# Kernel tuning notes

Measured on AMD Instinct MI355X. Metric: run time of the kernel, lower is better.

Reference implementation:

```python
import jax, jax.numpy as jnp
import numpy as np

B, S, D = 16, 2048, 128

def setup_inputs() -> dict:
    key = jax.random.key(0)
    kq, kk, kv, km = jax.random.split(key, 4)
    Q = jax.random.normal(kq, (B, S, D), dtype=jnp.float32)
    K = jax.random.normal(kk, (B, S, D), dtype=jnp.float32)
    V = jax.random.normal(kv, (B, S, D), dtype=jnp.float32)
    # mask: True entries are masked out (filled with -inf), same as torch.masked_fill_
    mask = jax.random.randint(km, (B, S, S), 0, 2).astype(bool)
    return {"Q": Q, "K": K, "V": V, "mask": mask, "dk": 128}

def reference(Q, K, V, mask, dk):
    # scores: [B, S_q, S_k]
    w = jnp.einsum('bqd,bkd->bqk', Q, K)
    w = jnp.where(mask, -jnp.inf, w)
    # scale applied to masked scores (as in original: mask first, then divide);
    # -inf / scale stays -inf, so math matches exactly.
    scale = jnp.asarray(dk, w.dtype) ** 0.5
    p = jax.nn.softmax(w / scale, axis=-1)
    # context: [B, S_q, D]
    return jnp.einsum('bqk,bkd->bqd', p, V)
```

## Files before the change

### kernel.cpp

```cpp
#include <hip/hip_runtime.h>
#include <hip/hip_bf16.h>
#include <stdint.h>

typedef __attribute__((ext_vector_type(8)))  short short8;
typedef __attribute__((ext_vector_type(4)))  float floatx4;
typedef __attribute__((ext_vector_type(16))) float floatx16;

#define S_LEN 2048
#define DH    128
#define BQ    64
#define BKV   64
#define NSTEP (S_LEN / BKV)
#define SCALE 0.08838834764831845f
#define SCALE2 0.12753785429791905f
#define DTHR 11.541560327111708f

__device__ __forceinline__ float ex2(float x) { return __builtin_amdgcn_exp2f(x); }

__device__ __forceinline__ unsigned short f2b(float f) {
    union { float f; unsigned u; } v; v.f = f;
    unsigned r = v.u + 0x7fffu + ((v.u >> 16) & 1u);
    return (unsigned short)(r >> 16);
}

__device__ __forceinline__ unsigned cvt_pk(float lo, float hi) {
    unsigned r;
    asm("v_cvt_pk_bf16_f32 %0, %1, %2" : "=v"(r) : "v"(lo), "v"(hi));
    return r;
}

__device__ __forceinline__ void gll16(const void* g, void* l) {
    __builtin_amdgcn_global_load_lds(
        (__attribute__((address_space(1))) void*)(g),
        (__attribute__((address_space(3))) void*)(l), 16, 0, 0);
}


__global__ __launch_bounds__(256) void conv_k(const float* __restrict__ K,
                                              unsigned short* __restrict__ Kbf)
{
    int i = blockIdx.x * 256 + threadIdx.x;
    float4 v = ((const float4*)K)[i];
    ushort4 o;
    o.x = f2b(v.x); o.y = f2b(v.y); o.z = f2b(v.z); o.w = f2b(v.w);
    ((ushort4*)Kbf)[i] = o;
}

__global__ __launch_bounds__(256) void transp_v(const float* __restrict__ V,
                                                unsigned short* __restrict__ Vt)
{
    __shared__ float t[32][33];
    const int k0 = blockIdx.x * 32, d0 = blockIdx.y * 32, b = blockIdx.z;
    const int tx = threadIdx.x & 31, ty = threadIdx.x >> 5;
    const float* Vb = V + ((size_t)b * S_LEN + k0) * DH + d0;
    #pragma unroll
    for (int i = 0; i < 4; ++i)
        t[ty + 8 * i][tx] = Vb[(size_t)(ty + 8 * i) * DH + tx];
    __syncthreads();
    unsigned short* Vtb = Vt + ((size_t)b * DH + d0) * S_LEN + k0;
    #pragma unroll
    for (int i = 0; i < 4; ++i)
        Vtb[(size_t)(ty + 8 * i) * S_LEN + tx] = f2b(t[tx][ty + 8 * i]);
}

__global__ __launch_bounds__(256) void pack_mask(const int* __restrict__ M,
                                                 unsigned long long* __restrict__ P)
{
    const int lane = threadIdx.x & 63;
    const int wv   = threadIdx.x >> 6;
    const int row  = blockIdx.x * 4 + wv;
    const int* Mr  = M + (size_t)row * S_LEN;
    unsigned long long* Pr = P + (size_t)row * 32;
    #pragma unroll
    for (int it = 0; it < 8; ++it) {
        int4 v = *(const int4*)(Mr + it * 256 + lane * 4);
        unsigned long long b0 = __ballot(v.x != 0);
        unsigned long long b1 = __ballot(v.y != 0);
        unsigned long long b2 = __ballot(v.z != 0);
        unsigned long long b3 = __ballot(v.w != 0);
        if (lane == 0) {
            Pr[it * 4 + 0] = b0;
            Pr[it * 4 + 1] = b1;
            Pr[it * 4 + 2] = b2;
            Pr[it * 4 + 3] = b3;
        }
    }
}

#define LDS_BYTES 69632

__global__ __launch_bounds__(256, 2)
void attn_fwd(const float* __restrict__ Q, const unsigned short* __restrict__ Kbf,
              const unsigned short* __restrict__ Vt,
              const unsigned long long* __restrict__ Pm,
              float* __restrict__ O)
{
    __shared__ __align__(128) char lds[LDS_BYTES];

    const int tid  = threadIdx.x;
    const int lane = tid & 63;
    const int w    = tid >> 6;
    const int wq   = w & 1;
    const int wk   = w >> 1;
    const int lq   = lane & 31;
    const int hi   = lane >> 5;
    const int qt   = blockIdx.x;
    const int b    = blockIdx.y;
    const int q0   = qt * BQ;

    const int vd = tid & 127;
    const int vh = tid >> 7;
    const int krow_l = lane >> 4;
    const int kcol_l = (lane & 15) * 16;

    short8 qf[8];
    {
        const float* qrow = Q + ((size_t)(b * S_LEN + q0 + wq * 32 + lq)) * DH;
        #pragma unroll
        for (int dsub = 0; dsub < 8; ++dsub) {
            const float* p = qrow + dsub * 16 + hi * 8;
            float4 a  = *(const float4*)(p);
            float4 bb = *(const float4*)(p + 4);
            short8 f;
            f[0] = f2b(a.x * SCALE2);  f[1] = f2b(a.y * SCALE2);
            f[2] = f2b(a.z * SCALE2);  f[3] = f2b(a.w * SCALE2);
            f[4] = f2b(bb.x * SCALE2); f[5] = f2b(bb.y * SCALE2);
            f[6] = f2b(bb.z * SCALE2); f[7] = f2b(bb.w * SCALE2);
            qf[dsub] = f;
        }
    }

    float m_run = -1e30f;
    float l_run = 0.f;
    floatx16 accO[4];
    #pragma unroll
    for (int i = 0; i < 4; ++i) accO[i] = (floatx16)(0.f);

    const char*           Kb8 = (const char*)(Kbf + (size_t)b * S_LEN * DH);
    const unsigned short* Vtb = Vt + (size_t)b * DH * S_LEN;
    const unsigned long long* Pk = Pm
        + ((size_t)(b * S_LEN + q0 + wq * 32 + lq) << 5);

    short8 vreg[4];
    unsigned long long mgc[4], mgn[4];

#define LOAD_MG(DST, G) {                                                     \
    ulonglong2 a_ = *(const ulonglong2*)(Pk + (G) * 4);                       \
    ulonglong2 b_ = *(const ulonglong2*)(Pk + (G) * 4 + 2);                   \
    DST[0] = a_.x; DST[1] = a_.y; DST[2] = b_.x; DST[3] = b_.y; }

    #pragma unroll
    for (int i = 0; i < 4; ++i) {
        int j = (w << 2) | i;
        int r = 4 * j + krow_l;
        unsigned cb = (unsigned)kcol_l ^ (unsigned)((r & 15) << 4);
        gll16(Kb8 + (size_t)r * 256 + cb, lds + j * 1024);
    }
    #pragma unroll
    for (int j = 0; j < 4; ++j)
        vreg[j] = *(const short8*)(Vtb + (size_t)vd * S_LEN + vh * 32 + j * 8);
    #pragma unroll
    for (int j = 0; j < 4; ++j)
        *(short8*)(lds + 32768 + vd * 144 + vh * 64 + j * 16) = vreg[j];
    #pragma unroll
    for (int j = 0; j < 4; ++j)
        vreg[j] = *(const short8*)(Vtb + (size_t)vd * S_LEN + BKV + vh * 32 + j * 8);
    LOAD_MG(mgc, 0);
    LOAD_MG(mgn, 1);
    __syncthreads();

#define STEP_BODY(T, TT) {                                                    \
    const int pb  = (T) & 1;                                                  \
    const int kv0 = (T) * BKV;                                                \
                                                  \
    if ((T) + 1 < NSTEP) {                                                    \
        const char* Ksrc = Kb8 + (size_t)(kv0 + BKV) * 256;                   \
        char* KHn = lds + ((pb ^ 1) * 16384);                                 \
        _Pragma("unroll")                                                     \
        for (int i = 0; i < 4; ++i) {                                         \
            int j = (w << 2) | i;                                             \
            int r = 4 * j + krow_l;                                           \
            unsigned cb = (unsigned)kcol_l ^ (unsigned)((r & 15) << 4);       \
            gll16(Ksrc + (size_t)r * 256 + cb, KHn + j * 1024);               \
        }                                                                     \
    }                                                                         \
                            \
    if ((T) + 1 < NSTEP) {                                                    \
        _Pragma("unroll")                                                     \
        for (int j = 0; j < 4; ++j)                                           \
            *(short8*)(lds + 32768 + (pb ^ 1) * 18432 + vd * 144 + vh * 64    \
                       + j * 16) = vreg[j];                                   \
    }                                                                         \
    if ((T) + 2 < NSTEP) {                                                    \
        const unsigned short* vs_ = Vtb + (size_t)vd * S_LEN                  \
                                   + (kv0 + 2 * BKV) + vh * 32;               \
        _Pragma("unroll")                                                     \
        for (int j = 0; j < 4; ++j)                                           \
            vreg[j] = *(const short8*)(vs_ + j * 8);                          \
    }                                                                         \
            \
    floatx16 accS = (floatx16)(0.f);                                          \
    {                                                                         \
        const char* KHp = lds + pb * 16384;                                   \
        const int krow = wk * 32 + lq;                                        \
        const char* kbase = KHp + krow * 256;                                 \
        const unsigned ksw = (unsigned)((krow & 15) << 4);                    \
        __builtin_amdgcn_s_setprio(1);                                        \
        _Pragma("unroll")                                                     \
        for (int dsub = 0; dsub < 8; ++dsub) {                                \
            short8 kf = *(const short8*)(kbase +                              \
                ((unsigned)(dsub * 32 + hi * 16) ^ ksw));                     \
            accS = __builtin_amdgcn_mfma_f32_32x32x16_bf16(                   \
                       kf, qf[dsub], accS, 0, 0, 0);                          \
        }                                                                     \
        __builtin_amdgcn_s_setprio(0);                                        \
    }                                                                         \
                               \
    const int base_ = (TT) * 16 + wk * 8 + hi;                                \
    unsigned mb0 = (unsigned)(mgc[0] >> base_);                               \
    unsigned mb1 = (unsigned)(mgc[1] >> base_);                               \
    unsigned mb2 = (unsigned)(mgc[2] >> base_);                               \
    unsigned mb3 = (unsigned)(mgc[3] >> base_);                               \
    float p_[16];                                                             \
    _Pragma("unroll")                                                         \
    for (int j = 0; j < 4; ++j) {                                             \
        p_[4*j+0] = ((mb0 >> (2*j)) & 1u) ? -1e30f : accS[4*j+0];             \
        p_[4*j+1] = ((mb1 >> (2*j)) & 1u) ? -1e30f : accS[4*j+1];             \
        p_[4*j+2] = ((mb2 >> (2*j)) & 1u) ? -1e30f : accS[4*j+2];             \
        p_[4*j+3] = ((mb3 >> (2*j)) & 1u) ? -1e30f : accS[4*j+3];             \
    }                                                                         \
    float mx = p_[0];                                                         \
    _Pragma("unroll")                                                         \
    for (int r = 1; r < 16; ++r) mx = fmaxf(mx, p_[r]);                       \
    mx = fmaxf(mx, __shfl_xor(mx, 32));                                       \
    int need = __any(mx - m_run > DTHR);                                      \
    float corr = 1.0f;                                                        \
    if (need) {                                                               \
        float mn = fmaxf(m_run, mx);                                          \
        corr = ex2(m_run - mn);                                               \
        m_run = mn;                                                           \
    }                                                                         \
    float ts = 0.f;                                                           \
    _Pragma("unroll")                                                         \
    for (int r = 0; r < 16; ++r) { p_[r] = ex2(p_[r] - m_run); ts += p_[r]; } \
    ts += __shfl_xor(ts, 32);                                                 \
    if (need) {                                                               \
        l_run = l_run * corr + ts;                                            \
        _Pragma("unroll")                                                     \
        for (int ds = 0; ds < 4; ++ds) {                                      \
            floatx16 o = accO[ds];                                            \
            _Pragma("unroll")                                                 \
            for (int r = 0; r < 16; ++r) o[r] *= corr;                        \
            accO[ds] = o;                                                     \
        }                                                                     \
    } else {                                                                  \
        l_run += ts;                                                          \
    }                                                                         \
              \
    short8 pf[2];                                                             \
    _Pragma("unroll")                                                         \
    for (int ks = 0; ks < 2; ++ks) {                                          \
        unsigned a01 = cvt_pk(p_[8*ks+0], p_[8*ks+1]);                        \
        unsigned a23 = cvt_pk(p_[8*ks+2], p_[8*ks+3]);                        \
        unsigned b01 = cvt_pk(p_[8*ks+4], p_[8*ks+5]);                        \
        unsigned b23 = cvt_pk(p_[8*ks+6], p_[8*ks+7]);                        \
        unsigned ta01 = (unsigned)__shfl_xor((int)a01, 32);                   \
        unsigned ta23 = (unsigned)__shfl_xor((int)a23, 32);                   \
        unsigned tb01 = (unsigned)__shfl_xor((int)b01, 32);                   \
        unsigned tb23 = (unsigned)__shfl_xor((int)b23, 32);                   \
        union { unsigned u[4]; short8 v; } pu;                                \
        pu.u[0] = hi ? tb01 : a01;                                            \
        pu.u[1] = hi ? tb23 : a23;                                            \
        pu.u[2] = hi ? b01 : ta01;                                            \
        pu.u[3] = hi ? b23 : ta23;                                            \
        pf[ks] = pu.v;                                                        \
    }                                                                         \
           \
    {                                                                         \
        const char* VTp = lds + 32768 + pb * 18432;                           \
        __builtin_amdgcn_s_setprio(1);                                        \
        _Pragma("unroll")                                                     \
        for (int ds = 0; ds < 4; ++ds) {                                      \
            const char* vbase = VTp + (ds * 32 + lq) * 144 + wk * 64 + hi*16; \
            _Pragma("unroll")                                                 \
            for (int ks = 0; ks < 2; ++ks) {                                  \
                short8 vf = *(const short8*)(vbase + ks * 32);                \
                accO[ds] = __builtin_amdgcn_mfma_f32_32x32x16_bf16(           \
                               vf, pf[ks], accO[ds], 0, 0, 0);                \
            }                                                                 \
        }                                                                     \
        __builtin_amdgcn_s_setprio(0);                                        \
    }                                                                         \
    __syncthreads(); }

    for (int g = 0; g < 8; ++g) {
        STEP_BODY(4 * g + 0, 0)
        STEP_BODY(4 * g + 1, 1)
        STEP_BODY(4 * g + 2, 2)
        STEP_BODY(4 * g + 3, 3)
        mgc[0] = mgn[0]; mgc[1] = mgn[1]; mgc[2] = mgn[2]; mgc[3] = mgn[3];
        if (g + 2 < 8) LOAD_MG(mgn, g + 2);
    }
#undef STEP_BODY
#undef LOAD_MG

    {
        float* mg = (float*)lds;
        const int slot = (wq * 64 + lane) * 68;
        if (wk == 1) {
            #pragma unroll
            for (int ds = 0; ds < 4; ++ds)
                #pragma unroll
                for (int rr = 0; rr < 4; ++rr) {
                    float4 v;
                    v.x = accO[ds][4*rr+0]; v.y = accO[ds][4*rr+1];
                    v.z = accO[ds][4*rr+2]; v.w = accO[ds][4*rr+3];
                    *(float4*)(mg + slot + ds * 16 + rr * 4) = v;
                }
            mg[slot + 64] = m_run;
            mg[slot + 65] = l_run;
        }
        __syncthreads();
        if (wk == 0) {
            float m1 = mg[slot + 64], l1 = mg[slot + 65];
            float m  = fmaxf(m_run, m1);
            float f0 = ex2(m_run - m), f1 = ex2(m1 - m);
            float l  = l_run * f0 + l1 * f1;
            float inv = (l > 0.f) ? 1.f / l : 0.f;
            float* Ob = O + ((size_t)(b * S_LEN + q0 + wq * 32 + lq)) * DH;
            #pragma unroll
            for (int ds = 0; ds < 4; ++ds)
                #pragma unroll
                for (int rr = 0; rr < 4; ++rr) {
                    float4 part = *(const float4*)(mg + slot + ds * 16 + rr * 4);
                    float4 ov;
                    ov.x = (accO[ds][4*rr+0] * f0 + part.x * f1) * inv;
                    ov.y = (accO[ds][4*rr+1] * f0 + part.y * f1) * inv;
                    ov.z = (accO[ds][4*rr+2] * f0 + part.z * f1) * inv;
                    ov.w = (accO[ds][4*rr+3] * f0 + part.w * f1) * inv;
                    *(float4*)(Ob + ds * 32 + 8 * rr + 4 * hi) = ov;
                }
        }
    }
}

#define FB_LDS_BYTES 77824

__global__ __launch_bounds__(256, 2)
void attn_fwd_fb(const float* __restrict__ Q, const float* __restrict__ K,
                 const float* __restrict__ V, const int* __restrict__ M,
                 float* __restrict__ O)
{
    __shared__ __align__(128) char lds[FB_LDS_BYTES];

    const int tid  = threadIdx.x;
    const int lane = tid & 63;
    const int w    = tid >> 6;
    const int c    = lane & 15;
    const int g    = lane >> 4;
    const int qt   = blockIdx.x;
    const int b    = blockIdx.y;
    const int q0   = qt * 64;

    const int rbase = tid >> 5;
    const int c4    = tid & 31;
    const unsigned swk = (unsigned)(c4 * 8) ^ (unsigned)(rbase << 4);
    const int vd    = tid & 127;
    const int vk0   = (tid >> 7) * 32;

    short8 qf[4];
    {
        const float* qrow = Q + ((size_t)(b * S_LEN + q0 + w * 16 + c)) * DH;
        #pragma unroll
        for (int dk = 0; dk < 4; ++dk) {
            const float* p = qrow + dk * 32 + g * 8;
            float4 a  = *(const float4*)(p);
            float4 bb = *(const float4*)(p + 4);
            short8 f;
            f[0] = f2b(a.x * SCALE);  f[1] = f2b(a.y * SCALE);
            f[2] = f2b(a.z * SCALE);  f[3] = f2b(a.w * SCALE);
            f[4] = f2b(bb.x * SCALE); f[5] = f2b(bb.y * SCALE);
            f[6] = f2b(bb.z * SCALE); f[7] = f2b(bb.w * SCALE);
            qf[dk] = f;
        }
    }

    float m_run[4] = {-1e30f, -1e30f, -1e30f, -1e30f};
    float l_run[4] = {0.f, 0.f, 0.f, 0.f};
    floatx4 accO[8];
    #pragma unroll
    for (int i = 0; i < 8; ++i) accO[i] = (floatx4)(0.f);

    const float* Kb = K + (size_t)b * S_LEN * DH;
    const float* Vb = V + (size_t)b * S_LEN * DH;
    const int*   Mb = M + (size_t)b * S_LEN * S_LEN + (size_t)q0 * S_LEN;

    size_t moff[4];
    #pragma unroll
    for (int r = 0; r < 4; ++r)
        moff[r] = (size_t)(w * 16 + 4 * g + r) * S_LEN;

    float4 kreg[8];
    float  vreg[32];
    int    mreg[16];

    #pragma unroll
    for (int i = 0; i < 8; ++i)
        kreg[i] = *(const float4*)(Kb + (size_t)(i * 8 + rbase) * DH + c4 * 4);
    #pragma unroll
    for (int j = 0; j < 32; ++j)
        vreg[j] = Vb[(size_t)(vk0 + j) * DH + vd];
    #pragma unroll
    for (int r = 0; r < 4; ++r)
        #pragma unroll
        for (int n = 0; n < 4; ++n)
            mreg[r * 4 + n] = Mb[moff[r] + n * 16 + c];

    #pragma unroll
    for (int i = 0; i < 8; ++i) {
        float4 kv = kreg[i];
        unsigned long long kp =
              (unsigned long long)f2b(kv.x)
            | ((unsigned long long)f2b(kv.y) << 16)
            | ((unsigned long long)f2b(kv.z) << 32)
            | ((unsigned long long)f2b(kv.w) << 48);
        *(unsigned long long*)(lds + (i * 8 + rbase) * 256 + swk) = kp;
    }
    {
        char* vbase = lds + 32768 + vd * 144 + vk0 * 2;
        #pragma unroll
        for (int i = 0; i < 4; ++i) {
            short8 pk;
            #pragma unroll
            for (int e = 0; e < 8; ++e) pk[e] = f2b(vreg[i * 8 + e]);
            *(short8*)(vbase + i * 16) = pk;
        }
    }
    #pragma unroll
    for (int i = 0; i < 8; ++i)
        kreg[i] = *(const float4*)(Kb + (size_t)(BKV + i * 8 + rbase) * DH + c4 * 4);
    #pragma unroll
    for (int j = 0; j < 32; ++j)
        vreg[j] = Vb[(size_t)(BKV + vk0 + j) * DH + vd];

    __syncthreads();

    char* psw = lds + 69632 + w * 2048;

    for (int step = 0; step < NSTEP; ++step) {
        const int p = step & 1;
        const int kv0 = step * BKV;
        char* KHp = lds + p * 16384;
        char* VTp = lds + 32768 + p * 18432;

        floatx4 accS[4];
        #pragma unroll
        for (int n = 0; n < 4; ++n) accS[n] = (floatx4)(0.f);
        #pragma unroll
        for (int n = 0; n < 4; ++n) {
            const char* krow = KHp + (n * 16 + c) * 256;
            #pragma unroll
            for (int dk = 0; dk < 4; ++dk) {
                unsigned colb = (unsigned)(dk * 64 + g * 16) ^ (unsigned)((c & 7) << 4);
                short8 kf = *(const short8*)(krow + colb);
                accS[n] = __builtin_amdgcn_mfma_f32_16x16x32_bf16(qf[dk], kf, accS[n], 0, 0, 0);
            }
        }

        float pv[4][4];
        float corr[4];
        #pragma unroll
        for (int r = 0; r < 4; ++r) {
            float sv[4];
            #pragma unroll
            for (int n = 0; n < 4; ++n) {
                float s = accS[n][r];
                if (mreg[r * 4 + n]) s = -1e30f;
                sv[n] = s;
            }
            float tm = fmaxf(fmaxf(sv[0], sv[1]), fmaxf(sv[2], sv[3]));
            #pragma unroll
            for (int off = 1; off < 16; off <<= 1)
                tm = fmaxf(tm, __shfl_xor(tm, off, 64));
            float mn = fmaxf(m_run[r], tm);
            corr[r]  = __expf(m_run[r] - mn);
            m_run[r] = mn;
            float ts = 0.f;
            #pragma unroll
            for (int n = 0; n < 4; ++n) { pv[n][r] = __expf(sv[n] - mn); ts += pv[n][r]; }
            #pragma unroll
            for (int off = 1; off < 16; off <<= 1)
                ts += __shfl_xor(ts, off, 64);
            l_run[r] = l_run[r] * corr[r] + ts;
        }
        if (step + 1 < NSTEP) {
            const int kvn = kv0 + BKV;
            #pragma unroll
            for (int r = 0; r < 4; ++r)
                #pragma unroll
                for (int n = 0; n < 4; ++n)
                    mreg[r * 4 + n] = Mb[moff[r] + kvn + n * 16 + c];
        }

        #pragma unroll
        for (int s8 = 0; s8 < 8; ++s8) {
            floatx4 o = accO[s8];
            o[0] *= corr[0]; o[1] *= corr[1]; o[2] *= corr[2]; o[3] *= corr[3];
            accO[s8] = o;
        }

        #pragma unroll
        for (int r = 0; r < 4; ++r) {
            int rl = 4 * g + r;
            #pragma unroll
            for (int n = 0; n < 4; ++n) {
                unsigned colb = (unsigned)((n * 16 + c) * 2) ^ (unsigned)((rl & 7) << 4);
                *(unsigned short*)(psw + rl * 128 + colb) = f2b(pv[n][r]);
            }
        }

        #pragma unroll
        for (int sub = 0; sub < 2; ++sub) {
            unsigned colb = (unsigned)(sub * 64 + g * 16) ^ (unsigned)((c & 7) << 4);
            short8 pf = *(const short8*)(psw + c * 128 + colb);
            #pragma unroll
            for (int s8 = 0; s8 < 8; ++s8) {
                short8 vf = *(const short8*)(VTp + (s8 * 16 + c) * 144 + sub * 64 + g * 16);
                accO[s8] = __builtin_amdgcn_mfma_f32_16x16x32_bf16(pf, vf, accO[s8], 0, 0, 0);
            }
        }

        if (step + 1 < NSTEP) {
            char* KHn = lds + (p ^ 1) * 16384;
            char* VTn = lds + 32768 + (p ^ 1) * 18432;
            #pragma unroll
            for (int i = 0; i < 8; ++i) {
                float4 kv = kreg[i];
                unsigned long long kp =
                      (unsigned long long)f2b(kv.x)
                    | ((unsigned long long)f2b(kv.y) << 16)
                    | ((unsigned long long)f2b(kv.z) << 32)
                    | ((unsigned long long)f2b(kv.w) << 48);
                *(unsigned long long*)(KHn + (i * 8 + rbase) * 256 + swk) = kp;
            }
            char* vbase = VTn + vd * 144 + vk0 * 2;
            #pragma unroll
            for (int i = 0; i < 4; ++i) {
                short8 pk;
                #pragma unroll
                for (int e = 0; e < 8; ++e) pk[e] = f2b(vreg[i * 8 + e]);
                *(short8*)(vbase + i * 16) = pk;
            }
            if (step + 2 < NSTEP) {
                const int kvn2 = kv0 + 2 * BKV;
                #pragma unroll
                for (int i = 0; i < 8; ++i)
                    kreg[i] = *(const float4*)(Kb + (size_t)(kvn2 + i * 8 + rbase) * DH + c4 * 4);
                #pragma unroll
                for (int j = 0; j < 32; ++j)
                    vreg[j] = Vb[(size_t)(kvn2 + vk0 + j) * DH + vd];
            }
        }
        __syncthreads();
    }

    float inv[4];
    #pragma unroll
    for (int r = 0; r < 4; ++r) inv[r] = (l_run[r] > 0.f) ? 1.f / l_run[r] : 0.f;
    float* Ob = O + ((size_t)(b * S_LEN + q0 + w * 16)) * DH;
    #pragma unroll
    for (int s8 = 0; s8 < 8; ++s8) {
        #pragma unroll
        for (int r = 0; r < 4; ++r) {
            Ob[(size_t)(4 * g + r) * DH + s8 * 16 + c] = accO[s8][r] * inv[r];
        }
    }
}

extern "C" void kernel_launch(void* const* d_in, const int* in_sizes, int n_in,
                              void* d_out, int out_size, void* d_ws, size_t ws_size,
                              hipStream_t stream) {
    const float* Q = (const float*)d_in[0];
    const float* K = (const float*)d_in[1];
    const float* V = (const float*)d_in[2];
    const int*   M = (const int*)d_in[3];
    float*       O = (float*)d_out;

    const size_t elems    = (size_t)16 * S_LEN * DH;
    const size_t kv_bytes = elems * sizeof(unsigned short);
    const size_t pm_bytes = (size_t)16 * S_LEN * 32 * 8;
    if (ws_size >= 2 * kv_bytes + pm_bytes) {
        unsigned short*     Kbf = (unsigned short*)d_ws;
        unsigned short*     Vt  = (unsigned short*)d_ws + elems;
        unsigned long long* Pm  = (unsigned long long*)((char*)d_ws + 2 * kv_bytes);
        conv_k<<<dim3((unsigned)(elems / 4 / 256)), dim3(256), 0, stream>>>(K, Kbf);
        transp_v<<<dim3(S_LEN / 32, DH / 32, 16), dim3(256), 0, stream>>>(V, Vt);
        pack_mask<<<dim3(16 * S_LEN / 4), dim3(256), 0, stream>>>(M, Pm);
        attn_fwd<<<dim3(S_LEN / BQ, 16), dim3(256), 0, stream>>>(Q, Kbf, Vt, Pm, O);
    } else {
        attn_fwd_fb<<<dim3(S_LEN / 64, 16), dim3(256), 0, stream>>>(Q, K, V, M, O);
    }
}
```

Measured before the change: 136.6 us.

## Pre-swizzle K and V into MFMA fragment layout and load directly to registers

The preprocessing kernels now write K and V in bf16, already arranged in the per-lane MFMA operand fragment order. The attention kernel loads these fragments straight from global memory into registers, with K double-buffered across steps. This removes the LDS staging buffers and the per-step __syncthreads, and halves the LDS footprint. In exchange, register pressure rises, the global (L2) fragment loads are now exposed inside the step, and each wave re-reads K/V fragments that were previously shared through LDS.

```diff
diff --git a/kernel.cpp b/kernel.cpp
--- a/kernel.cpp
+++ b/kernel.cpp
@@ -29,25 +29,28 @@
     return r;
 }
 
-__device__ __forceinline__ void gll16(const void* g, void* l) {
-    __builtin_amdgcn_global_load_lds(
-        (__attribute__((address_space(1))) void*)(g),
-        (__attribute__((address_space(3))) void*)(l), 16, 0, 0);
-}
-
-
-__global__ __launch_bounds__(256) void conv_k(const float* __restrict__ K,
-                                              unsigned short* __restrict__ Kbf)
+
+__global__ __launch_bounds__(256) void kfrag_make(const float* __restrict__ K,
+                                                  unsigned short* __restrict__ KF)
 {
-    int i = blockIdx.x * 256 + threadIdx.x;
-    float4 v = ((const float4*)K)[i];
-    ushort4 o;
-    o.x = f2b(v.x); o.y = f2b(v.y); o.z = f2b(v.z); o.w = f2b(v.w);
-    ((ushort4*)Kbf)[i] = o;
-}
-
-__global__ __launch_bounds__(256) void transp_v(const float* __restrict__ V,
-                                                unsigned short* __restrict__ Vt)
+    const int T = blockIdx.x, b = blockIdx.y;
+    const float* Kb = K + ((size_t)b * S_LEN + T * 64) * DH;
+    unsigned short* out = KF + ((size_t)(b * 32 + T)) * 1024 * 8;
+    #pragma unroll
+    for (int i = 0; i < 4; ++i) {
+        int F = i * 256 + threadIdx.x;
+        int lq = F & 31, h = (F >> 5) & 1, dsub = (F >> 6) & 7, wk = F >> 9;
+        const float* src = Kb + (size_t)(wk * 32 + lq) * DH + dsub * 16 + h * 8;
+        float4 a = *(const float4*)src, bb = *(const float4*)(src + 4);
+        short8 f;
+        f[0] = f2b(a.x);  f[1] = f2b(a.y);  f[2] = f2b(a.z);  f[3] = f2b(a.w);
+        f[4] = f2b(bb.x); f[5] = f2b(bb.y); f[6] = f2b(bb.z); f[7] = f2b(bb.w);
+        *(short8*)(out + (size_t)F * 8) = f;
+    }
+}
+
+__global__ __launch_bounds__(256) void vfrag_make(const float* __restrict__ V,
+                                                  unsigned short* __restrict__ VF)
 {
     __shared__ float t[32][33];
     const int k0 = blockIdx.x * 32, d0 = blockIdx.y * 32, b = blockIdx.z;
@@ -57,10 +60,19 @@
     for (int i = 0; i < 4; ++i)
         t[ty + 8 * i][tx] = Vb[(size_t)(ty + 8 * i) * DH + tx];
     __syncthreads();
-    unsigned short* Vtb = Vt + ((size_t)b * DH + d0) * S_LEN + k0;
-    #pragma unroll
-    for (int i = 0; i < 4; ++i)
-        Vtb[(size_t)(ty + 8 * i) * S_LEN + tx] = f2b(t[tx][ty + 8 * i]);
+    if (threadIdx.x < 128) {
+        const int lq = threadIdx.x & 31;
+        const int h  = (threadIdx.x >> 5) & 1;
+        const int ks = threadIdx.x >> 6;
+        const int T = k0 >> 6, wk = (k0 >> 5) & 1, ds = d0 >> 5;
+        short8 f;
+        #pragma unroll
+        for (int e = 0; e < 8; ++e)
+            f[e] = f2b(t[ks * 16 + h * 8 + e][lq]);
+        unsigned short* o = VF +
+            ((((((size_t)(b * 32 + T) * 4 + ds) * 2 + wk) * 2 + ks) * 2 + h) * 32 + lq) * 8;
+        *(short8*)o = f;
+    }
 }
 
 __global__ __launch_bounds__(256) void pack_mask(const int* __restrict__ M,
@@ -87,11 +99,11 @@
     }
 }
 
-#define LDS_BYTES 69632
+#define LDS_BYTES 34816
 
 __global__ __launch_bounds__(256, 2)
-void attn_fwd(const float* __restrict__ Q, const unsigned short* __restrict__ Kbf,
-              const unsigned short* __restrict__ Vt,
+void attn_fwd(const float* __restrict__ Q, const unsigned short* __restrict__ KF,
+              const unsigned short* __restrict__ VF,
               const unsigned long long* __restrict__ Pm,
               float* __restrict__ O)
 {
@@ -108,11 +120,6 @@
     const int b    = blockIdx.y;
     const int q0   = qt * BQ;
 
-    const int vd = tid & 127;
-    const int vh = tid >> 7;
-    const int krow_l = lane >> 4;
-    const int kcol_l = (lane & 15) * 16;
-
     short8 qf[8];
     {
         const float* qrow = Q + ((size_t)(b * S_LEN + q0 + wq * 32 + lq)) * DH;
@@ -136,86 +143,54 @@
     #pragma unroll
     for (int i = 0; i < 4; ++i) accO[i] = (floatx16)(0.f);
 
-    const char*           Kb8 = (const char*)(Kbf + (size_t)b * S_LEN * DH);
-    const unsigned short* Vtb = Vt + (size_t)b * DH * S_LEN;
+    const unsigned short* KFl = KF + (((size_t)(b * 32) * 2 + wk) * 512
+                                      + (size_t)hi * 32 + lq) * 8;
+    const unsigned short* VFl = VF + ((((size_t)(b * 32) * 4 * 2 + wk) * 2) * 2 * 32
+                                      + (size_t)hi * 32 + lq) * 8;
+
     const unsigned long long* Pk = Pm
         + ((size_t)(b * S_LEN + q0 + wq * 32 + lq) << 5);
 
-    short8 vreg[4];
     unsigned long long mgc[4], mgn[4];
+    short8 kfA[8], kfB[8], vfc[8];
 
 #define LOAD_MG(DST, G) {                                                     \
     ulonglong2 a_ = *(const ulonglong2*)(Pk + (G) * 4);                       \
     ulonglong2 b_ = *(const ulonglong2*)(Pk + (G) * 4 + 2);                   \
     DST[0] = a_.x; DST[1] = a_.y; DST[2] = b_.x; DST[3] = b_.y; }
 
-    #pragma unroll
-    for (int i = 0; i < 4; ++i) {
-        int j = (w << 2) | i;
-        int r = 4 * j + krow_l;
-        unsigned cb = (unsigned)kcol_l ^ (unsigned)((r & 15) << 4);
-        gll16(Kb8 + (size_t)r * 256 + cb, lds + j * 1024);
-    }
-    #pragma unroll
-    for (int j = 0; j < 4; ++j)
-        vreg[j] = *(const short8*)(Vtb + (size_t)vd * S_LEN + vh * 32 + j * 8);
-    #pragma unroll
-    for (int j = 0; j < 4; ++j)
-        *(short8*)(lds + 32768 + vd * 144 + vh * 64 + j * 16) = vreg[j];
-    #pragma unroll
-    for (int j = 0; j < 4; ++j)
-        vreg[j] = *(const short8*)(Vtb + (size_t)vd * S_LEN + BKV + vh * 32 + j * 8);
+#define LOAD_KF(DST, T) {                                                     \
+    const unsigned short* kp_ = KFl + (size_t)(T) * (2 * 512 * 8);            \
+    _Pragma("unroll")                                                         \
+    for (int dsub = 0; dsub < 8; ++dsub)                                      \
+        DST[dsub] = *(const short8*)(kp_ + dsub * 512);                       \
+}
+
+#define LOAD_VF(T) {                                                          \
+    _Pragma("unroll")                                                         \
+    for (int ds = 0; ds < 4; ++ds)                                            \
+        _Pragma("unroll")                                                     \
+        for (int ks = 0; ks < 2; ++ks)                                        \
+            vfc[ds * 2 + ks] = *(const short8*)(VFl                           \
+                + ((size_t)(T) * 16 + ds * 4 + ks) * (2 * 32 * 8));           \
+}
+
+    LOAD_KF(kfA, 0);
     LOAD_MG(mgc, 0);
     LOAD_MG(mgn, 1);
-    __syncthreads();
-
-#define STEP_BODY(T, TT) {                                                    \
-    const int pb  = (T) & 1;                                                  \
-    const int kv0 = (T) * BKV;                                                \
-                                                  \
-    if ((T) + 1 < NSTEP) {                                                    \
-        const char* Ksrc = Kb8 + (size_t)(kv0 + BKV) * 256;                   \
-        char* KHn = lds + ((pb ^ 1) * 16384);                                 \
-        _Pragma("unroll")                                                     \
-        for (int i = 0; i < 4; ++i) {                                         \
-            int j = (w << 2) | i;                                             \
-            int r = 4 * j + krow_l;                                           \
-            unsigned cb = (unsigned)kcol_l ^ (unsigned)((r & 15) << 4);       \
-            gll16(Ksrc + (size_t)r * 256 + cb, KHn + j * 1024);               \
-        }                                                                     \
-    }                                                                         \
-                            \
-    if ((T) + 1 < NSTEP) {                                                    \
-        _Pragma("unroll")                                                     \
-        for (int j = 0; j < 4; ++j)                                           \
-            *(short8*)(lds + 32768 + (pb ^ 1) * 18432 + vd * 144 + vh * 64    \
-                       + j * 16) = vreg[j];                                   \
-    }                                                                         \
-    if ((T) + 2 < NSTEP) {                                                    \
-        const unsigned short* vs_ = Vtb + (size_t)vd * S_LEN                  \
-                                   + (kv0 + 2 * BKV) + vh * 32;               \
-        _Pragma("unroll")                                                     \
-        for (int j = 0; j < 4; ++j)                                           \
-            vreg[j] = *(const short8*)(vs_ + j * 8);                          \
-    }                                                                         \
-            \
+
+#define STEP_BODY(T, TT, KFC, KFN) {                                          \
+    if ((T) + 1 < NSTEP) LOAD_KF(KFN, (T) + 1);                               \
+    LOAD_VF(T);                                                               \
+                                                                    \
     floatx16 accS = (floatx16)(0.f);                                          \
-    {                                                                         \
-        const char* KHp = lds + pb * 16384;                                   \
-        const int krow = wk * 32 + lq;                                        \
-        const char* kbase = KHp + krow * 256;                                 \
-        const unsigned ksw = (unsigned)((krow & 15) << 4);                    \
-        __builtin_amdgcn_s_setprio(1);                                        \
-        _Pragma("unroll")                                                     \
-        for (int dsub = 0; dsub < 8; ++dsub) {                                \
-            short8 kf = *(const short8*)(kbase +                              \
-                ((unsigned)(dsub * 32 + hi * 16) ^ ksw));                     \
-            accS = __builtin_amdgcn_mfma_f32_32x32x16_bf16(                   \
-                       kf, qf[dsub], accS, 0, 0, 0);                          \
-        }                                                                     \
-        __builtin_amdgcn_s_setprio(0);                                        \
-    }                                                                         \
-                               \
+    __builtin_amdgcn_s_setprio(1);                                            \
+    _Pragma("unroll")                                                         \
+    for (int dsub = 0; dsub < 8; ++dsub)                                      \
+        accS = __builtin_amdgcn_mfma_f32_32x32x16_bf16(                       \
+                   KFC[dsub], qf[dsub], accS, 0, 0, 0);                       \
+    __builtin_amdgcn_s_setprio(0);                                            \
+                                           \
     const int base_ = (TT) * 16 + wk * 8 + hi;                                \
     unsigned mb0 = (unsigned)(mgc[0] >> base_);                               \
     unsigned mb1 = (unsigned)(mgc[1] >> base_);                               \
@@ -256,7 +231,7 @@
     } else {                                                                  \
         l_run += ts;                                                          \
     }                                                                         \
-              \
+                                 \
     short8 pf[2];                                                             \
     _Pragma("unroll")                                                         \
     for (int ks = 0; ks < 2; ++ks) {                                          \
@@ -275,33 +250,28 @@
         pu.u[3] = hi ? b23 : ta23;                                            \
         pf[ks] = pu.v;                                                        \
     }                                                                         \
-           \
-    {                                                                         \
-        const char* VTp = lds + 32768 + pb * 18432;                           \
-        __builtin_amdgcn_s_setprio(1);                                        \
+                                                                      \
+    __builtin_amdgcn_s_setprio(1);                                            \
+    _Pragma("unroll")                                                         \
+    for (int ds = 0; ds < 4; ++ds)                                            \
         _Pragma("unroll")                                                     \
-        for (int ds = 0; ds < 4; ++ds) {                                      \
-            const char* vbase = VTp + (ds * 32 + lq) * 144 + wk * 64 + hi*16; \
-            _Pragma("unroll")                                                 \
-            for (int ks = 0; ks < 2; ++ks) {                                  \
-                short8 vf = *(const short8*)(vbase + ks * 32);                \
-                accO[ds] = __builtin_amdgcn_mfma_f32_32x32x16_bf16(           \
-                               vf, pf[ks], accO[ds], 0, 0, 0);                \
-            }                                                                 \
-        }                                                                     \
-        __builtin_amdgcn_s_setprio(0);                                        \
-    }                                                                         \
-    __syncthreads(); }
+        for (int ks = 0; ks < 2; ++ks)                                        \
+            accO[ds] = __builtin_amdgcn_mfma_f32_32x32x16_bf16(               \
+                           vfc[ds * 2 + ks], pf[ks], accO[ds], 0, 0, 0);      \
+    __builtin_amdgcn_s_setprio(0);                                            \
+}
 
     for (int g = 0; g < 8; ++g) {
-        STEP_BODY(4 * g + 0, 0)
-        STEP_BODY(4 * g + 1, 1)
-        STEP_BODY(4 * g + 2, 2)
-        STEP_BODY(4 * g + 3, 3)
+        STEP_BODY(4 * g + 0, 0, kfA, kfB)
+        STEP_BODY(4 * g + 1, 1, kfB, kfA)
+        STEP_BODY(4 * g + 2, 2, kfA, kfB)
+        STEP_BODY(4 * g + 3, 3, kfB, kfA)
         mgc[0] = mgn[0]; mgc[1] = mgn[1]; mgc[2] = mgn[2]; mgc[3] = mgn[3];
         if (g + 2 < 8) LOAD_MG(mgn, g + 2);
     }
 #undef STEP_BODY
+#undef LOAD_KF
+#undef LOAD_VF
 #undef LOAD_MG
 
     {
@@ -590,13 +560,13 @@
     const size_t kv_bytes = elems * sizeof(unsigned short);
     const size_t pm_bytes = (size_t)16 * S_LEN * 32 * 8;
     if (ws_size >= 2 * kv_bytes + pm_bytes) {
-        unsigned short*     Kbf = (unsigned short*)d_ws;
-        unsigned short*     Vt  = (unsigned short*)d_ws + elems;
-        unsigned long long* Pm  = (unsigned long long*)((char*)d_ws + 2 * kv_bytes);
-        conv_k<<<dim3((unsigned)(elems / 4 / 256)), dim3(256), 0, stream>>>(K, Kbf);
-        transp_v<<<dim3(S_LEN / 32, DH / 32, 16), dim3(256), 0, stream>>>(V, Vt);
+        unsigned short*     KF = (unsigned short*)d_ws;
+        unsigned short*     VF = (unsigned short*)d_ws + elems;
+        unsigned long long* Pm = (unsigned long long*)((char*)d_ws + 2 * kv_bytes);
+        kfrag_make<<<dim3(32, 16), dim3(256), 0, stream>>>(K, KF);
+        vfrag_make<<<dim3(S_LEN / 32, DH / 32, 16), dim3(256), 0, stream>>>(V, VF);
         pack_mask<<<dim3(16 * S_LEN / 4), dim3(256), 0, stream>>>(M, Pm);
-        attn_fwd<<<dim3(S_LEN / BQ, 16), dim3(256), 0, stream>>>(Q, Kbf, Vt, Pm, O);
+        attn_fwd<<<dim3(S_LEN / BQ, 16), dim3(256), 0, stream>>>(Q, KF, VF, Pm, O);
     } else {
         attn_fwd_fb<<<dim3(S_LEN / 64, 16), dim3(256), 0, stream>>>(Q, K, V, M, O);
     }
```

Result: faster. 123.5 us (-9.6%).
